# Optimization experiments

Hardware: AMD Instinct MI355X
Metric: run time of the kernel (lower is better)

Reference implementation:

```python
import jax, jax.numpy as jnp
import numpy as np
from jax.ops import segment_sum

N_NODES = 100000


def gcn_conv(x, edge_index, W, b, n_nodes):
    # PyG GCNConv: add self-loops, symmetric normalization, linear, scatter-add, bias
    src = jnp.concatenate([edge_index[0], jnp.arange(n_nodes, dtype=edge_index.dtype)])
    dst = jnp.concatenate([edge_index[1], jnp.arange(n_nodes, dtype=edge_index.dtype)])
    deg = segment_sum(jnp.ones(src.shape[0], dtype=x.dtype), dst, num_segments=n_nodes)
    dinv = jnp.where(deg > 0, jax.lax.rsqrt(deg), 0.0)
    norm = dinv[src] * dinv[dst]            # [E+N]
    h = x @ W                               # [N, out] dense GEMM first (PyG order)
    msg = h[src] * norm[:, None]            # gather + scale, [E+N, out]
    out = segment_sum(msg, dst, num_segments=n_nodes)  # scatter-add
    return out + b


def setup_inputs() -> dict:
    key = jax.random.key(0)
    k1, k2, k3, k4, k5, k6 = jax.random.split(key, 6)
    in_c, hid_c, out_c = 128, 128, 64
    n_edges = 1600000
    x = jax.random.normal(k1, (N_NODES, in_c), dtype=jnp.float32)
    edge_index = jax.random.randint(k2, (2, n_edges), 0, N_NODES, dtype=jnp.int64)
    # Glorot-ish init for weights, zeros for bias (PyG defaults)
    W1 = jax.random.normal(k3, (in_c, hid_c), dtype=jnp.float32) / np.sqrt(in_c)
    b1 = jnp.zeros((hid_c,), dtype=jnp.float32)
    W2 = jax.random.normal(k4, (hid_c, out_c), dtype=jnp.float32) / np.sqrt(hid_c)
    b2 = jnp.zeros((out_c,), dtype=jnp.float32)
    return {"x": x, "edge_index": edge_index, "W1": W1, "b1": b1, "W2": W2, "b2": b2}


def reference(x, edge_index, W1, b1, W2, b2):
    h = gcn_conv(x, edge_index, W1, b1, N_NODES)
    h = jax.nn.relu(h)
    out = gcn_conv(h, edge_index, W2, b2, N_NODES)
    return out
```

## Files before the change

### kernel.cpp

```cpp
#include <hip/hip_runtime.h>
#include <hip/hip_fp16.h>

#define NN 100000
#define NBKT 196
#define BCAP 16384

using f16x8 = __attribute__((ext_vector_type(8))) _Float16;
using f32x4 = __attribute__((ext_vector_type(4))) float;

__device__ __forceinline__ void fma4(float4& a, float s, const float4& w) {
  a.x = fmaf(s, w.x, a.x);
  a.y = fmaf(s, w.y, a.y);
  a.z = fmaf(s, w.z, a.z);
  a.w = fmaf(s, w.w, a.w);
}

__device__ __forceinline__ void add8(float* a, uint4 q) {
  const __half2* p = (const __half2*)&q;
#pragma unroll
  for (int j = 0; j < 4; ++j) {
    float2 f = __half22float2(p[j]);
    a[2 * j]     += f.x;
    a[2 * j + 1] += f.y;
  }
}

__device__ __forceinline__ unsigned packh2(float x, float y) {
  __half2 h = __floats2half2_rn(x, y);
  return *(unsigned*)&h;
}

__global__ __launch_bounds__(256) void k_binA(const int* __restrict__ e,
                                              const float* __restrict__ W1,
                                              const float* __restrict__ W2,
                                              _Float16* __restrict__ wt1,
                                              _Float16* __restrict__ wt2,
                                              int* __restrict__ gcur,
                                              unsigned int* __restrict__ tmp,
                                              int E, int nA) {
  const int b = blockIdx.x;
  const int tid = threadIdx.x;
  if (b >= nA) {
    int wb = b - nA;
    if (wb < 64) {
      int i = wb * 256 + tid;
      int n = i >> 7, k = i & 127;
      wt1[i] = (_Float16)W1[k * 128 + n];
    } else {
      int i = (wb - 64) * 256 + tid;
      int n = i >> 7, k = i & 127;
      wt2[i] = (_Float16)W2[k * 64 + n];
    }
    return;
  }
  __shared__ int cnt[256];
  __shared__ int pcur[256];
  __shared__ int sm_flag;
  cnt[tid] = 0;
  if (tid < 64) {
    int n64 = E < 64 ? E : 64;
    int odd = (tid < n64) ? e[2 * tid + 1] : 0;
    unsigned long long nz = __ballot(odd != 0);
    if (tid == 0) sm_flag = (nz == 0ull) ? 1 : 0;
  }
  __syncthreads();
  const int m = sm_flag;
  const bool pok = ((E & 1) == 0);
  const int start = b * 4096;
  int ss[16], dd[16];
#pragma unroll
  for (int k = 0; k < 8; ++k) {
    int i = start + 2 * (tid + k * 256);
    int s0 = -1, s1 = -1, d0 = 0, d1 = 0;
    if (i < E) {
      if (m) {
        if (pok) {
          int4 sp = ((const int4*)e)[i >> 1];
          int4 dp = ((const int4*)e)[(E + i) >> 1];
          s0 = sp.x; s1 = sp.z; d0 = dp.x; d1 = dp.z;
        } else {
          s0 = (int)((const long long*)e)[i];
          d0 = (int)((const long long*)e)[E + i];
          if (i + 1 < E) {
            s1 = (int)((const long long*)e)[i + 1];
            d1 = (int)((const long long*)e)[E + i + 1];
          }
        }
      } else {
        if (pok) {
          int2 sp = ((const int2*)e)[i >> 1];
          int2 dp = ((const int2*)(e + E))[i >> 1];
          s0 = sp.x; s1 = sp.y; d0 = dp.x; d1 = dp.y;
        } else {
          s0 = e[i]; d0 = e[E + i];
          if (i + 1 < E) { s1 = e[i + 1]; d1 = e[E + i + 1]; }
        }
      }
      if (i + 1 >= E) s1 = -1;
      atomicAdd(&cnt[d0 >> 9], 1);
      if (s1 >= 0) atomicAdd(&cnt[d1 >> 9], 1);
    }
    ss[2 * k] = s0; dd[2 * k] = d0;
    ss[2 * k + 1] = s1; dd[2 * k + 1] = d1;
  }
  __syncthreads();
  if (tid < NBKT && cnt[tid] > 0)
    pcur[tid] = tid * BCAP + atomicAdd(&gcur[tid], cnt[tid]);
  __syncthreads();
#pragma unroll
  for (int k = 0; k < 16; ++k) {
    if (ss[k] >= 0) {
      int bk = dd[k] >> 9;
      int p = atomicAdd(&pcur[bk], 1);
      tmp[p] = ((unsigned)ss[k] << 9) | (unsigned)(dd[k] & 511);
    }
  }
}

__global__ __launch_bounds__(256) void k_binB(const unsigned int* __restrict__ tmp,
                                              const int* __restrict__ gcur,
                                              int* __restrict__ rowptr,
                                              float* __restrict__ dinv,
                                              int* __restrict__ srcs) {
  __shared__ int sbuf[256];
  __shared__ int hist[512];
  __shared__ int lofs[512];
  const int b = blockIdx.x;
  const int tid = threadIdx.x;
  int c = (tid < NBKT) ? gcur[tid] : 0;
  sbuf[tid] = c;
  __syncthreads();
#pragma unroll
  for (int off = 1; off < 256; off <<= 1) {
    int t = (tid >= off) ? sbuf[tid - off] : 0;
    __syncthreads();
    sbuf[tid] += t;
    __syncthreads();
  }
  const int total = sbuf[255];
  const int incl = sbuf[b];
  const int base_b = (b > 0) ? sbuf[b - 1] : 0;
  const int cntb = incl - base_b;
  if (b == 0 && tid == 0) rowptr[NN] = total;
  __syncthreads();
  hist[tid] = 0;
  hist[tid + 256] = 0;
  __syncthreads();
  const int tbeg = b * BCAP;
  const int tend = tbeg + cntb;
  for (int j = tbeg + tid; j < tend; j += 256) atomicAdd(&hist[tmp[j] & 511], 1);
  __syncthreads();
  int a0 = hist[2 * tid], a1 = hist[2 * tid + 1];
  int sv = a0 + a1;
  sbuf[tid] = sv;
  __syncthreads();
#pragma unroll
  for (int off = 1; off < 256; off <<= 1) {
    int t = (tid >= off) ? sbuf[tid - off] : 0;
    __syncthreads();
    sbuf[tid] += t;
    __syncthreads();
  }
  int excl = sbuf[tid] - sv;
  lofs[2 * tid] = excl;
  lofs[2 * tid + 1] = excl + a0;
  __syncthreads();
  for (int i = tid; i < 512; i += 256) {
    int node = (b << 9) + i;
    if (node < NN) {
      rowptr[node] = base_b + lofs[i];
      dinv[node] = rsqrtf((float)(hist[i] + 1));
    }
  }
  __syncthreads();
  for (int j = tbeg + tid; j < tend; j += 256) {
    unsigned v = tmp[j];
    int p = base_b + atomicAdd(&lofs[v & 511], 1);
    srcs[p] = (int)(v >> 9);
  }
}

template <int N, bool AHALF>
__global__ __launch_bounds__(256) void k_gemm_mfma(const void* __restrict__ Av,
                                                   const _Float16* __restrict__ Wt,
                                                   const float* __restrict__ dinv,
                                                   _Float16* __restrict__ out, int M) {
  constexpr int NF = N / 16;
  __shared__ _Float16 As[64 * 136];
  __shared__ _Float16 Bs[N * 136];
  const int tid = threadIdx.x;
  const long long row0 = (long long)blockIdx.x * 64;
  if (AHALF) {
    const _Float16* A = (const _Float16*)Av;
#pragma unroll
    for (int t = 0; t < 4; ++t) {
      int i = tid + t * 256;
      int m = i >> 4, q = i & 15;
      long long row = row0 + m;
      uint4 v = make_uint4(0, 0, 0, 0);
      if (row < M) v = ((const uint4*)A)[row * 16 + q];
      *(uint4*)&As[m * 136 + q * 8] = v;
    }
  } else {
    const float* A = (const float*)Av;
#pragma unroll
    for (int t = 0; t < 8; ++t) {
      int i = tid + t * 256;
      int m = i >> 5, q = i & 31;
      long long row = row0 + m;
      float4 v = make_float4(0.f, 0.f, 0.f, 0.f);
      if (row < M) v = ((const float4*)A)[row * 32 + q];
      uint2 w2 = make_uint2(packh2(v.x, v.y), packh2(v.z, v.w));
      *(uint2*)&As[m * 136 + q * 4] = w2;
    }
  }
#pragma unroll
  for (int t = 0; t < N / 16; ++t) {
    int i = tid + t * 256;
    int n = i >> 4, q = i & 15;
    uint4 v = ((const uint4*)Wt)[i];
    *(uint4*)&Bs[n * 136 + q * 8] = v;
  }
  __syncthreads();
  const int lane = tid & 63;
  const int wrow = (tid >> 6) * 16;
  const int r = lane & 15, g = lane >> 4;
  f32x4 acc[NF] = {};
#pragma unroll
  for (int ks = 0; ks < 4; ++ks) {
    f16x8 av = *(const f16x8*)&As[(wrow + r) * 136 + ks * 32 + g * 8];
#pragma unroll
    for (int cf = 0; cf < NF; ++cf) {
      f16x8 bv = *(const f16x8*)&Bs[(cf * 16 + r) * 136 + ks * 32 + g * 8];
      acc[cf] = __builtin_amdgcn_mfma_f32_16x16x32_f16(av, bv, acc[cf], 0, 0, 0);
    }
  }
#pragma unroll
  for (int q = 0; q < 4; ++q) {
    long long row = row0 + wrow + g * 4 + q;
    if (row < M) {
      float sc = dinv[row];
#pragma unroll
      for (int cf = 0; cf < NF; ++cf)
        out[row * N + cf * 16 + r] = (_Float16)(sc * acc[cf][q]);
    }
  }
}

template <int C, bool RELU16>
__global__ __launch_bounds__(256) void k_gather_s(const int* __restrict__ rowptr,
                                                  const int* __restrict__ srcs,
                                                  const float* __restrict__ dinv,
                                                  const _Float16* __restrict__ h,
                                                  const float* __restrict__ b,
                                                  void* __restrict__ outv) {
  constexpr int LPN = C / 8;
  constexpr int NPW = 64 / LPN;
  constexpr int NPB = NPW * 4;
  const int wave = threadIdx.x >> 6;
  const int lane = threadIdx.x & 63;
  const int grp = lane / LPN;
  const int li = lane % LPN;
  const int node = blockIdx.x * NPB + wave * NPW + grp;
  if (node >= NN) return;
  const float dd = dinv[node];
  float acc[8];
  {
    uint4 q = *(const uint4*)(h + (long long)node * C + li * 8);
    const __half2* p = (const __half2*)&q;
#pragma unroll
    for (int j = 0; j < 4; ++j) {
      float2 f = __half22float2(p[j]);
      acc[2 * j]     = f.x;
      acc[2 * j + 1] = f.y;
    }
  }
  const int beg = rowptr[node], end = rowptr[node + 1];
  int e = beg;
  for (; e + 4 <= end; e += 4) {
    int s0 = srcs[e], s1 = srcs[e + 1], s2 = srcs[e + 2], s3 = srcs[e + 3];
    uint4 q0 = *(const uint4*)(h + (long long)s0 * C + li * 8);
    uint4 q1 = *(const uint4*)(h + (long long)s1 * C + li * 8);
    uint4 q2 = *(const uint4*)(h + (long long)s2 * C + li * 8);
    uint4 q3 = *(const uint4*)(h + (long long)s3 * C + li * 8);
    add8(acc, q0);
    add8(acc, q1);
    add8(acc, q2);
    add8(acc, q3);
  }
  for (; e < end; ++e) {
    uint4 q0 = *(const uint4*)(h + (long long)srcs[e] * C + li * 8);
    add8(acc, q0);
  }
  const float4* b4 = (const float4*)b;
  float4 bb0 = b4[li * 2], bb1 = b4[li * 2 + 1];
  float o[8];
  o[0] = fmaf(dd, acc[0], bb0.x);
  o[1] = fmaf(dd, acc[1], bb0.y);
  o[2] = fmaf(dd, acc[2], bb0.z);
  o[3] = fmaf(dd, acc[3], bb0.w);
  o[4] = fmaf(dd, acc[4], bb1.x);
  o[5] = fmaf(dd, acc[5], bb1.y);
  o[6] = fmaf(dd, acc[6], bb1.z);
  o[7] = fmaf(dd, acc[7], bb1.w);
  if (RELU16) {
#pragma unroll
    for (int j = 0; j < 8; ++j) o[j] = fmaxf(o[j], 0.f);
    uint4 w;
    w.x = packh2(o[0], o[1]);
    w.y = packh2(o[2], o[3]);
    w.z = packh2(o[4], o[5]);
    w.w = packh2(o[6], o[7]);
    *(uint4*)((_Float16*)outv + (long long)node * C + li * 8) = w;
  } else {
    float4* op = (float4*)((float*)outv + (long long)node * C + li * 8);
    op[0] = make_float4(o[0], o[1], o[2], o[3]);
    op[1] = make_float4(o[4], o[5], o[6], o[7]);
  }
}

__global__ void k_zero_i32(int* p, int n) {
  int i = blockIdx.x * 256 + threadIdx.x;
  if (i < n) p[i] = 0;
}

__global__ void k_detect_f(const int* __restrict__ e, int* flag, int E) {
  if (threadIdx.x == 0 && blockIdx.x == 0) {
    int n = E < 64 ? E : 64;
    int m = 1;
    for (int i = 0; i < n; ++i)
      if (e[2 * i + 1] != 0) { m = 0; break; }
    *flag = m;
  }
}

__global__ void k_deg_count(const int* __restrict__ e, const int* __restrict__ flag,
                            int* __restrict__ deg, int E) {
  int i = blockIdx.x * 256 + threadIdx.x;
  if (i >= E) return;
  int m = *flag;
  int d = m ? e[2 * (E + i)] : e[E + i];
  atomicAdd(&deg[d], 1);
}

__global__ void k_dinv_f(const int* __restrict__ deg, float* __restrict__ dinv) {
  int i = blockIdx.x * 256 + threadIdx.x;
  if (i < NN) dinv[i] = rsqrtf((float)(deg[i] + 1));
}

template <int N, bool RELU>
__global__ __launch_bounds__(256) void k_gemm_v(const float* __restrict__ A,
                                                const float* __restrict__ W,
                                                float* __restrict__ out, int M) {
  constexpr int K4 = 32;
  constexpr int N4 = N / 4;
  constexpr int CG = N4;
  constexpr int ROWS = (256 / CG) * 4;
  __shared__ float4 Wl[128 * N4];
  __shared__ float4 Xl[ROWS * K4];
  const int tid = threadIdx.x;
  const float4* W4 = (const float4*)W;
  for (int i = tid; i < 128 * N4; i += 256) Wl[i] = W4[i];
  const long long row0 = (long long)blockIdx.x * ROWS;
  const float4* A4 = (const float4*)A;
  for (int i = tid; i < ROWS * K4; i += 256) {
    int r = i >> 5;
    long long row = row0 + r;
    float4 v = make_float4(0.f, 0.f, 0.f, 0.f);
    if (row < M) v = A4[row * K4 + (i & 31)];
    if (RELU) {
      v.x = fmaxf(v.x, 0.f); v.y = fmaxf(v.y, 0.f);
      v.z = fmaxf(v.z, 0.f); v.w = fmaxf(v.w, 0.f);
    }
    Xl[i] = v;
  }
  __syncthreads();
  const int c = tid % CG;
  const int rb = (tid / CG) * 4;
  float4 a0 = make_float4(0, 0, 0, 0), a1 = a0, a2 = a0, a3 = a0;
#pragma unroll 4
  for (int k4 = 0; k4 < K4; ++k4) {
    float4 w0 = Wl[(k4 * 4 + 0) * N4 + c];
    float4 w1 = Wl[(k4 * 4 + 1) * N4 + c];
    float4 w2 = Wl[(k4 * 4 + 2) * N4 + c];
    float4 w3 = Wl[(k4 * 4 + 3) * N4 + c];
    float4 x0 = Xl[(rb + 0) * K4 + k4];
    float4 x1 = Xl[(rb + 1) * K4 + k4];
    float4 x2 = Xl[(rb + 2) * K4 + k4];
    float4 x3 = Xl[(rb + 3) * K4 + k4];
    fma4(a0, x0.x, w0); fma4(a0, x0.y, w1); fma4(a0, x0.z, w2); fma4(a0, x0.w, w3);
    fma4(a1, x1.x, w0); fma4(a1, x1.y, w1); fma4(a1, x1.z, w2); fma4(a1, x1.w, w3);
    fma4(a2, x2.x, w0); fma4(a2, x2.y, w1); fma4(a2, x2.z, w2); fma4(a2, x2.w, w3);
    fma4(a3, x3.x, w0); fma4(a3, x3.y, w1); fma4(a3, x3.z, w2); fma4(a3, x3.w, w3);
  }
  float4* O4 = (float4*)out;
  long long row = row0 + rb;
  if (row + 0 < M) O4[(row + 0) * N4 + c] = a0;
  if (row + 1 < M) O4[(row + 1) * N4 + c] = a1;
  if (row + 2 < M) O4[(row + 2) * N4 + c] = a2;
  if (row + 3 < M) O4[(row + 3) * N4 + c] = a3;
}

template <int C>
__global__ void k_self_bias(const float* __restrict__ h, const float* __restrict__ dinv,
                            const float* __restrict__ b, float* __restrict__ out) {
  constexpr int C4 = C / 4;
  int gid = blockIdx.x * 256 + threadIdx.x;
  if (gid >= NN * C4) return;
  int node = gid / C4;
  int cq = gid % C4;
  float di = dinv[node];
  float sc = di * di;
  float4 v = ((const float4*)h)[gid];
  float4 bb = ((const float4*)b)[cq];
  float4 o;
  o.x = fmaf(v.x, sc, bb.x);
  o.y = fmaf(v.y, sc, bb.y);
  o.z = fmaf(v.z, sc, bb.z);
  o.w = fmaf(v.w, sc, bb.w);
  ((float4*)out)[gid] = o;
}

template <int C>
__global__ void k_scatter(const int* __restrict__ e, const int* __restrict__ flag,
                          const float* __restrict__ dinv, const float* __restrict__ h,
                          float* __restrict__ out, int E) {
  constexpr int TPE = C / 4;
  long long gid = (long long)blockIdx.x * blockDim.x + threadIdx.x;
  int ei = (int)(gid / TPE);
  int cq = (int)(gid % TPE);
  if (ei >= E) return;
  int m = *flag;
  int s, d;
  if (m) { s = e[2 * ei]; d = e[2 * (E + ei)]; }
  else   { s = e[ei];     d = e[E + ei]; }
  float nrm = dinv[s] * dinv[d];
  float4 v = ((const float4*)h)[(long long)s * TPE + cq];
  float* op = out + (long long)d * C + (long long)cq * 4;
  unsafeAtomicAdd(op + 0, v.x * nrm);
  unsafeAtomicAdd(op + 1, v.y * nrm);
  unsafeAtomicAdd(op + 2, v.z * nrm);
  unsafeAtomicAdd(op + 3, v.w * nrm);
}

extern "C" void kernel_launch(void* const* d_in, const int* in_sizes, int n_in,
                              void* d_out, int out_size, void* d_ws, size_t ws_size,
                              hipStream_t stream) {
  const float* x  = (const float*)d_in[0];
  const int*   e  = (const int*)d_in[1];
  const float* W1 = (const float*)d_in[2];
  const float* b1 = (const float*)d_in[3];
  const float* W2 = (const float*)d_in[4];
  const float* b2 = (const float*)d_in[5];
  float* out = (float*)d_out;
  const int E = in_sizes[1] / 2;

  char* ws = (char*)d_ws;
  const size_t o_flag    = 0;
  const size_t o_dinv    = 16;
  const size_t o_rowptr  = 400016;
  const size_t o_gcur    = 800032;
  const size_t o_tmp     = 800832;
  const size_t o_srcs    = 13645888;
  const size_t o_wt1     = 20045888;
  const size_t o_wt2     = 20078656;
  const size_t o_h       = 20095040;
  const size_t o_out1    = 45695040;
  const size_t need_csr  = 71295040;

  int*      flag   = (int*)(ws + o_flag);
  float*    dinv   = (float*)(ws + o_dinv);
  int*      rowptr = (int*)(ws + o_rowptr);
  int*      gcur   = (int*)(ws + o_gcur);
  unsigned* tmp    = (unsigned*)(ws + o_tmp);
  int*      srcs   = (int*)(ws + o_srcs);
  _Float16* wt1    = (_Float16*)(ws + o_wt1);
  _Float16* wt2    = (_Float16*)(ws + o_wt2);
  _Float16* hh     = (_Float16*)(ws + o_h);
  _Float16* out1   = (_Float16*)(ws + o_out1);

  if (ws_size >= need_csr) {
    const int nA = (E + 4095) / 4096;
    hipMemsetAsync(gcur, 0, NBKT * sizeof(int), stream);
    k_binA<<<nA + 96, 256, 0, stream>>>(e, W1, W2, wt1, wt2, gcur, tmp, E, nA);
    k_binB<<<NBKT, 256, 0, stream>>>(tmp, gcur, rowptr, dinv, srcs);

    k_gemm_mfma<128, false><<<(NN + 63) / 64, 256, 0, stream>>>(x, wt1, dinv, hh, NN);
    k_gather_s<128, true><<<(NN + 15) / 16, 256, 0, stream>>>(rowptr, srcs, dinv, hh, b1, out1);

    k_gemm_mfma<64, true><<<(NN + 63) / 64, 256, 0, stream>>>(out1, wt2, dinv, hh, NN);
    k_gather_s<64, false><<<(NN + 31) / 32, 256, 0, stream>>>(rowptr, srcs, dinv, hh, b2, out);
  } else {
    int*   deg   = (int*)(ws + 400016);
    float* hF    = (float*)(ws + (1 << 20));
    float* out1F = (float*)(ws + (1 << 20) + 51200000);
    k_detect_f<<<1, 64, 0, stream>>>(e, flag, E);
    k_zero_i32<<<(NN + 255) / 256, 256, 0, stream>>>(deg, NN);
    k_deg_count<<<(E + 255) / 256, 256, 0, stream>>>(e, flag, deg, E);
    k_dinv_f<<<(NN + 255) / 256, 256, 0, stream>>>(deg, dinv);
    k_gemm_v<128, false><<<(NN + 31) / 32, 256, 0, stream>>>(x, W1, hF, NN);
    k_self_bias<128><<<(NN * 32 + 255) / 256, 256, 0, stream>>>(hF, dinv, b1, out1F);
    long long tot1 = (long long)E * 32;
    k_scatter<128><<<(int)((tot1 + 255) / 256), 256, 0, stream>>>(e, flag, dinv, hF, out1F, E);
    k_gemm_v<64, true><<<(NN + 63) / 64, 256, 0, stream>>>(out1F, W2, hF, NN);
    k_self_bias<64><<<(NN * 16 + 255) / 256, 256, 0, stream>>>(hF, dinv, b2, out);
    long long tot2 = (long long)E * 16;
    k_scatter<64><<<(int)((tot2 + 255) / 256), 256, 0, stream>>>(e, flag, dinv, hF, out, E);
  }
}
```

Measured before the change: 222.7 us.

## Store features in 16-column slices so gathers hit a smaller working set

The GEMM output and the layer-1 hidden features are now stored as 16-channel column slices, each a contiguous [NN,16] half array. The gather kernel launches one block group per slice, with 2 lanes per node, so each pass over the edges touches only a 3.2MB slice that can stay in cache instead of the full feature matrix. Index loads and output stores now use nontemporal hints. In exchange, the CSR index list is read once per slice (8x or 4x more index traffic), and the GEMM writes become more scattered.

```diff
diff --git a/kernel.cpp b/kernel.cpp
--- a/kernel.cpp
+++ b/kernel.cpp
@@ -4,9 +4,11 @@
 #define NN 100000
 #define NBKT 196
 #define BCAP 16384
+#define SLST (NN * 16)
 
 using f16x8 = __attribute__((ext_vector_type(8))) _Float16;
 using f32x4 = __attribute__((ext_vector_type(4))) float;
+using u32x4 = __attribute__((ext_vector_type(4))) unsigned;
 
 __device__ __forceinline__ void fma4(float4& a, float s, const float4& w) {
   a.x = fmaf(s, w.x, a.x);
@@ -198,7 +200,8 @@
       int m = i >> 4, q = i & 15;
       long long row = row0 + m;
       uint4 v = make_uint4(0, 0, 0, 0);
-      if (row < M) v = ((const uint4*)A)[row * 16 + q];
+      if (row < M)
+        v = *(const uint4*)(A + (size_t)(q >> 1) * SLST + row * 16 + (q & 1) * 8);
       *(uint4*)&As[m * 136 + q * 8] = v;
     }
   } else {
@@ -242,31 +245,33 @@
       float sc = dinv[row];
 #pragma unroll
       for (int cf = 0; cf < NF; ++cf)
-        out[row * N + cf * 16 + r] = (_Float16)(sc * acc[cf][q]);
+        out[(size_t)cf * SLST + row * 16 + r] = (_Float16)(sc * acc[cf][q]);
     }
   }
 }
 
 template <int C, bool RELU16>
-__global__ __launch_bounds__(256) void k_gather_s(const int* __restrict__ rowptr,
-                                                  const int* __restrict__ srcs,
-                                                  const float* __restrict__ dinv,
-                                                  const _Float16* __restrict__ h,
-                                                  const float* __restrict__ b,
-                                                  void* __restrict__ outv) {
-  constexpr int LPN = C / 8;
-  constexpr int NPW = 64 / LPN;
-  constexpr int NPB = NPW * 4;
-  const int wave = threadIdx.x >> 6;
-  const int lane = threadIdx.x & 63;
-  const int grp = lane / LPN;
-  const int li = lane % LPN;
-  const int node = blockIdx.x * NPB + wave * NPW + grp;
+__global__ __launch_bounds__(256) void k_gather_sl(const int* __restrict__ rowptr,
+                                                   const int* __restrict__ srcs,
+                                                   const float* __restrict__ dinv,
+                                                   const _Float16* __restrict__ h,
+                                                   const float* __restrict__ b,
+                                                   void* __restrict__ outv) {
+  constexpr int NSL = C / 16;
+  const int tid = threadIdx.x;
+  const int sl = (int)(blockIdx.x % NSL);
+  const int nb = (int)(blockIdx.x / NSL);
+  const int lane = tid & 63;
+  const int wave = tid >> 6;
+  const int grp = lane >> 1;
+  const int li = lane & 1;
+  const int node = nb * 128 + wave * 32 + grp;
   if (node >= NN) return;
+  const _Float16* hs = h + (size_t)sl * SLST;
   const float dd = dinv[node];
   float acc[8];
   {
-    uint4 q = *(const uint4*)(h + (long long)node * C + li * 8);
+    uint4 q = *(const uint4*)(hs + node * 16 + li * 8);
     const __half2* p = (const __half2*)&q;
 #pragma unroll
     for (int j = 0; j < 4; ++j) {
@@ -278,22 +283,27 @@
   const int beg = rowptr[node], end = rowptr[node + 1];
   int e = beg;
   for (; e + 4 <= end; e += 4) {
-    int s0 = srcs[e], s1 = srcs[e + 1], s2 = srcs[e + 2], s3 = srcs[e + 3];
-    uint4 q0 = *(const uint4*)(h + (long long)s0 * C + li * 8);
-    uint4 q1 = *(const uint4*)(h + (long long)s1 * C + li * 8);
-    uint4 q2 = *(const uint4*)(h + (long long)s2 * C + li * 8);
-    uint4 q3 = *(const uint4*)(h + (long long)s3 * C + li * 8);
+    int s0 = __builtin_nontemporal_load(srcs + e);
+    int s1 = __builtin_nontemporal_load(srcs + e + 1);
+    int s2 = __builtin_nontemporal_load(srcs + e + 2);
+    int s3 = __builtin_nontemporal_load(srcs + e + 3);
+    uint4 q0 = *(const uint4*)(hs + s0 * 16 + li * 8);
+    uint4 q1 = *(const uint4*)(hs + s1 * 16 + li * 8);
+    uint4 q2 = *(const uint4*)(hs + s2 * 16 + li * 8);
+    uint4 q3 = *(const uint4*)(hs + s3 * 16 + li * 8);
     add8(acc, q0);
     add8(acc, q1);
     add8(acc, q2);
     add8(acc, q3);
   }
   for (; e < end; ++e) {
-    uint4 q0 = *(const uint4*)(h + (long long)srcs[e] * C + li * 8);
+    int s0 = __builtin_nontemporal_load(srcs + e);
+    uint4 q0 = *(const uint4*)(hs + s0 * 16 + li * 8);
     add8(acc, q0);
   }
   const float4* b4 = (const float4*)b;
-  float4 bb0 = b4[li * 2], bb1 = b4[li * 2 + 1];
+  float4 bb0 = b4[sl * 4 + li * 2];
+  float4 bb1 = b4[sl * 4 + li * 2 + 1];
   float o[8];
   o[0] = fmaf(dd, acc[0], bb0.x);
   o[1] = fmaf(dd, acc[1], bb0.y);
@@ -306,16 +316,19 @@
   if (RELU16) {
 #pragma unroll
     for (int j = 0; j < 8; ++j) o[j] = fmaxf(o[j], 0.f);
-    uint4 w;
+    u32x4 w;
     w.x = packh2(o[0], o[1]);
     w.y = packh2(o[2], o[3]);
     w.z = packh2(o[4], o[5]);
     w.w = packh2(o[6], o[7]);
-    *(uint4*)((_Float16*)outv + (long long)node * C + li * 8) = w;
+    __builtin_nontemporal_store(
+        w, (u32x4*)((_Float16*)outv + (size_t)sl * SLST + node * 16 + li * 8));
   } else {
-    float4* op = (float4*)((float*)outv + (long long)node * C + li * 8);
-    op[0] = make_float4(o[0], o[1], o[2], o[3]);
-    op[1] = make_float4(o[4], o[5], o[6], o[7]);
+    float* op = (float*)outv + (size_t)node * C + sl * 16 + li * 8;
+    f32x4 v0 = {o[0], o[1], o[2], o[3]};
+    f32x4 v1 = {o[4], o[5], o[6], o[7]};
+    __builtin_nontemporal_store(v0, (f32x4*)op);
+    __builtin_nontemporal_store(v1, (f32x4*)(op + 4));
   }
 }
 
@@ -481,15 +494,16 @@
 
   if (ws_size >= need_csr) {
     const int nA = (E + 4095) / 4096;
-    hipMemsetAsync(gcur, 0, NBKT * sizeof(int), stream);
+    const int nNB = (NN + 127) / 128;
+    (void)hipMemsetAsync(gcur, 0, NBKT * sizeof(int), stream);
     k_binA<<<nA + 96, 256, 0, stream>>>(e, W1, W2, wt1, wt2, gcur, tmp, E, nA);
     k_binB<<<NBKT, 256, 0, stream>>>(tmp, gcur, rowptr, dinv, srcs);
 
     k_gemm_mfma<128, false><<<(NN + 63) / 64, 256, 0, stream>>>(x, wt1, dinv, hh, NN);
-    k_gather_s<128, true><<<(NN + 15) / 16, 256, 0, stream>>>(rowptr, srcs, dinv, hh, b1, out1);
+    k_gather_sl<128, true><<<nNB * 8, 256, 0, stream>>>(rowptr, srcs, dinv, hh, b1, out1);
 
     k_gemm_mfma<64, true><<<(NN + 63) / 64, 256, 0, stream>>>(out1, wt2, dinv, hh, NN);
-    k_gather_s<64, false><<<(NN + 31) / 32, 256, 0, stream>>>(rowptr, srcs, dinv, hh, b2, out);
+    k_gather_sl<64, false><<<nNB * 4, 256, 0, stream>>>(rowptr, srcs, dinv, hh, b2, out);
   } else {
     int*   deg   = (int*)(ws + 400016);
     float* hF    = (float*)(ws + (1 << 20));
```

Result: slower. 291.1 us (+30.7%).

## Fuse first GEMM into binning kernel and move degree scaling into gather

Applied to the files above, without the earlier changes.

The first GEMM no longer needs dinv, so it now runs as extra blocks of the edge-binning kernel, and that launch and the separate weight-transpose step disappear. The layer-1 gather instead applies dinv[src] per edge while it accumulates, which adds a random dinv load per edge. Weights are converted and transposed straight into shared memory inside each GEMM block. Nontemporal loads and stores are added for the srcs index stream and the gather outputs.

```diff
diff --git a/kernel.cpp b/kernel.cpp
--- a/kernel.cpp
+++ b/kernel.cpp
@@ -7,6 +7,7 @@
 
 using f16x8 = __attribute__((ext_vector_type(8))) _Float16;
 using f32x4 = __attribute__((ext_vector_type(4))) float;
+using u32x4 = __attribute__((ext_vector_type(4))) unsigned;
 
 __device__ __forceinline__ void fma4(float4& a, float s, const float4& w) {
   a.x = fmaf(s, w.x, a.x);
@@ -15,6 +16,16 @@
   a.w = fmaf(s, w.w, a.w);
 }
 
+__device__ __forceinline__ void acc8(float* a, float w, uint4 q) {
+  const __half2* p = (const __half2*)&q;
+#pragma unroll
+  for (int j = 0; j < 4; ++j) {
+    float2 f = __half22float2(p[j]);
+    a[2 * j]     = fmaf(w, f.x, a[2 * j]);
+    a[2 * j + 1] = fmaf(w, f.y, a[2 * j + 1]);
+  }
+}
+
 __device__ __forceinline__ void add8(float* a, uint4 q) {
   const __half2* p = (const __half2*)&q;
 #pragma unroll
@@ -30,41 +41,100 @@
   return *(unsigned*)&h;
 }
 
-__global__ __launch_bounds__(256) void k_binA(const int* __restrict__ e,
-                                              const float* __restrict__ W1,
-                                              const float* __restrict__ W2,
-                                              _Float16* __restrict__ wt1,
-                                              _Float16* __restrict__ wt2,
-                                              int* __restrict__ gcur,
-                                              unsigned int* __restrict__ tmp,
-                                              int E, int nA) {
+template <int N, bool AHALF, bool PRESCALE>
+__device__ __forceinline__ void gemm_body(int bid, const void* __restrict__ Av,
+                                          const float* __restrict__ W,
+                                          const float* __restrict__ dinv,
+                                          _Float16* __restrict__ out, int M,
+                                          _Float16* As, _Float16* Bs) {
+  constexpr int NF = N / 16;
+  const int tid = threadIdx.x;
+  const long long row0 = (long long)bid * 64;
+  if (AHALF) {
+    const _Float16* A = (const _Float16*)Av;
+#pragma unroll
+    for (int t = 0; t < 4; ++t) {
+      int i = tid + t * 256;
+      int m = i >> 4, q = i & 15;
+      long long row = row0 + m;
+      uint4 v = make_uint4(0, 0, 0, 0);
+      if (row < M) v = ((const uint4*)A)[row * 16 + q];
+      *(uint4*)&As[m * 136 + q * 8] = v;
+    }
+  } else {
+    const float* A = (const float*)Av;
+#pragma unroll
+    for (int t = 0; t < 8; ++t) {
+      int i = tid + t * 256;
+      int m = i >> 5, q = i & 31;
+      long long row = row0 + m;
+      float4 v = make_float4(0.f, 0.f, 0.f, 0.f);
+      if (row < M) v = ((const float4*)A)[row * 32 + q];
+      uint2 w2 = make_uint2(packh2(v.x, v.y), packh2(v.z, v.w));
+      *(uint2*)&As[m * 136 + q * 4] = w2;
+    }
+  }
+#pragma unroll
+  for (int t = 0; t < N / 2; ++t) {
+    int idx = tid + t * 256;
+    int k = idx / N, n = idx % N;
+    Bs[n * 136 + k] = (_Float16)W[idx];
+  }
+  __syncthreads();
+  const int lane = tid & 63;
+  const int wrow = (tid >> 6) * 16;
+  const int r = lane & 15, g = lane >> 4;
+  f32x4 acc[NF] = {};
+#pragma unroll
+  for (int ks = 0; ks < 4; ++ks) {
+    f16x8 av = *(const f16x8*)&As[(wrow + r) * 136 + ks * 32 + g * 8];
+#pragma unroll
+    for (int cf = 0; cf < NF; ++cf) {
+      f16x8 bv = *(const f16x8*)&Bs[(cf * 16 + r) * 136 + ks * 32 + g * 8];
+      acc[cf] = __builtin_amdgcn_mfma_f32_16x16x32_f16(av, bv, acc[cf], 0, 0, 0);
+    }
+  }
+#pragma unroll
+  for (int q = 0; q < 4; ++q) {
+    long long row = row0 + wrow + g * 4 + q;
+    if (row < M) {
+      float sc = PRESCALE ? dinv[row] : 1.0f;
+#pragma unroll
+      for (int cf = 0; cf < NF; ++cf)
+        out[row * N + cf * 16 + r] = (_Float16)(sc * acc[cf][q]);
+    }
+  }
+}
+
+__global__ __launch_bounds__(256) void k_binA_gemm(const int* __restrict__ e,
+                                                   int* __restrict__ gcur,
+                                                   unsigned int* __restrict__ tmp,
+                                                   int E, int nA,
+                                                   const float* __restrict__ x,
+                                                   const float* __restrict__ W1,
+                                                   _Float16* __restrict__ hh,
+                                                   int M) {
+  __shared__ char smem[52224];
   const int b = blockIdx.x;
   const int tid = threadIdx.x;
   if (b >= nA) {
-    int wb = b - nA;
-    if (wb < 64) {
-      int i = wb * 256 + tid;
-      int n = i >> 7, k = i & 127;
-      wt1[i] = (_Float16)W1[k * 128 + n];
-    } else {
-      int i = (wb - 64) * 256 + tid;
-      int n = i >> 7, k = i & 127;
-      wt2[i] = (_Float16)W2[k * 64 + n];
-    }
+    _Float16* As = (_Float16*)smem;
+    _Float16* Bs = (_Float16*)(smem + 64 * 136 * 2);
+    gemm_body<128, false, false>(b - nA, x, W1, nullptr, hh, M, As, Bs);
     return;
   }
-  __shared__ int cnt[256];
-  __shared__ int pcur[256];
-  __shared__ int sm_flag;
+  int* cnt = (int*)smem;
+  int* pcur = cnt + 256;
+  int* sm_flag = pcur + 256;
   cnt[tid] = 0;
   if (tid < 64) {
     int n64 = E < 64 ? E : 64;
     int odd = (tid < n64) ? e[2 * tid + 1] : 0;
     unsigned long long nz = __ballot(odd != 0);
-    if (tid == 0) sm_flag = (nz == 0ull) ? 1 : 0;
-  }
-  __syncthreads();
-  const int m = sm_flag;
+    if (tid == 0) *sm_flag = (nz == 0ull) ? 1 : 0;
+  }
+  __syncthreads();
+  const int m = *sm_flag;
   const bool pok = ((E & 1) == 0);
   const int start = b * 4096;
   int ss[16], dd[16];
@@ -117,6 +187,15 @@
   }
 }
 
+__global__ __launch_bounds__(256) void k_gemm2(const _Float16* __restrict__ A,
+                                               const float* __restrict__ W2,
+                                               const float* __restrict__ dinv,
+                                               _Float16* __restrict__ out, int M) {
+  __shared__ _Float16 As[64 * 136];
+  __shared__ _Float16 Bs[64 * 136];
+  gemm_body<64, true, true>(blockIdx.x, A, W2, dinv, out, M, As, Bs);
+}
+
 __global__ __launch_bounds__(256) void k_binB(const unsigned int* __restrict__ tmp,
                                               const int* __restrict__ gcur,
                                               int* __restrict__ rowptr,
@@ -180,88 +259,18 @@
   }
 }
 
-template <int N, bool AHALF>
-__global__ __launch_bounds__(256) void k_gemm_mfma(const void* __restrict__ Av,
-                                                   const _Float16* __restrict__ Wt,
-                                                   const float* __restrict__ dinv,
-                                                   _Float16* __restrict__ out, int M) {
-  constexpr int NF = N / 16;
-  __shared__ _Float16 As[64 * 136];
-  __shared__ _Float16 Bs[N * 136];
-  const int tid = threadIdx.x;
-  const long long row0 = (long long)blockIdx.x * 64;
-  if (AHALF) {
-    const _Float16* A = (const _Float16*)Av;
-#pragma unroll
-    for (int t = 0; t < 4; ++t) {
-      int i = tid + t * 256;
-      int m = i >> 4, q = i & 15;
-      long long row = row0 + m;
-      uint4 v = make_uint4(0, 0, 0, 0);
-      if (row < M) v = ((const uint4*)A)[row * 16 + q];
-      *(uint4*)&As[m * 136 + q * 8] = v;
-    }
-  } else {
-    const float* A = (const float*)Av;
-#pragma unroll
-    for (int t = 0; t < 8; ++t) {
-      int i = tid + t * 256;
-      int m = i >> 5, q = i & 31;
-      long long row = row0 + m;
-      float4 v = make_float4(0.f, 0.f, 0.f, 0.f);
-      if (row < M) v = ((const float4*)A)[row * 32 + q];
-      uint2 w2 = make_uint2(packh2(v.x, v.y), packh2(v.z, v.w));
-      *(uint2*)&As[m * 136 + q * 4] = w2;
-    }
-  }
-#pragma unroll
-  for (int t = 0; t < N / 16; ++t) {
-    int i = tid + t * 256;
-    int n = i >> 4, q = i & 15;
-    uint4 v = ((const uint4*)Wt)[i];
-    *(uint4*)&Bs[n * 136 + q * 8] = v;
-  }
-  __syncthreads();
-  const int lane = tid & 63;
-  const int wrow = (tid >> 6) * 16;
-  const int r = lane & 15, g = lane >> 4;
-  f32x4 acc[NF] = {};
-#pragma unroll
-  for (int ks = 0; ks < 4; ++ks) {
-    f16x8 av = *(const f16x8*)&As[(wrow + r) * 136 + ks * 32 + g * 8];
-#pragma unroll
-    for (int cf = 0; cf < NF; ++cf) {
-      f16x8 bv = *(const f16x8*)&Bs[(cf * 16 + r) * 136 + ks * 32 + g * 8];
-      acc[cf] = __builtin_amdgcn_mfma_f32_16x16x32_f16(av, bv, acc[cf], 0, 0, 0);
-    }
-  }
-#pragma unroll
-  for (int q = 0; q < 4; ++q) {
-    long long row = row0 + wrow + g * 4 + q;
-    if (row < M) {
-      float sc = dinv[row];
-#pragma unroll
-      for (int cf = 0; cf < NF; ++cf)
-        out[row * N + cf * 16 + r] = (_Float16)(sc * acc[cf][q]);
-    }
-  }
-}
-
-template <int C, bool RELU16>
-__global__ __launch_bounds__(256) void k_gather_s(const int* __restrict__ rowptr,
-                                                  const int* __restrict__ srcs,
-                                                  const float* __restrict__ dinv,
-                                                  const _Float16* __restrict__ h,
-                                                  const float* __restrict__ b,
-                                                  void* __restrict__ outv) {
-  constexpr int LPN = C / 8;
-  constexpr int NPW = 64 / LPN;
-  constexpr int NPB = NPW * 4;
+__global__ __launch_bounds__(256) void k_gather1(const int* __restrict__ rowptr,
+                                                 const int* __restrict__ srcs,
+                                                 const float* __restrict__ dinv,
+                                                 const _Float16* __restrict__ h,
+                                                 const float* __restrict__ b,
+                                                 _Float16* __restrict__ out) {
+  constexpr int C = 128;
   const int wave = threadIdx.x >> 6;
   const int lane = threadIdx.x & 63;
-  const int grp = lane / LPN;
-  const int li = lane % LPN;
-  const int node = blockIdx.x * NPB + wave * NPW + grp;
+  const int grp = lane >> 4;
+  const int li = lane & 15;
+  const int node = blockIdx.x * 16 + wave * 4 + grp;
   if (node >= NN) return;
   const float dd = dinv[node];
   float acc[8];
@@ -271,26 +280,32 @@
 #pragma unroll
     for (int j = 0; j < 4; ++j) {
       float2 f = __half22float2(p[j]);
-      acc[2 * j]     = f.x;
-      acc[2 * j + 1] = f.y;
+      acc[2 * j]     = dd * f.x;
+      acc[2 * j + 1] = dd * f.y;
     }
   }
   const int beg = rowptr[node], end = rowptr[node + 1];
   int e = beg;
   for (; e + 4 <= end; e += 4) {
-    int s0 = srcs[e], s1 = srcs[e + 1], s2 = srcs[e + 2], s3 = srcs[e + 3];
+    int s0 = __builtin_nontemporal_load(srcs + e);
+    int s1 = __builtin_nontemporal_load(srcs + e + 1);
+    int s2 = __builtin_nontemporal_load(srcs + e + 2);
+    int s3 = __builtin_nontemporal_load(srcs + e + 3);
+    float w0 = dinv[s0], w1 = dinv[s1], w2 = dinv[s2], w3 = dinv[s3];
     uint4 q0 = *(const uint4*)(h + (long long)s0 * C + li * 8);
     uint4 q1 = *(const uint4*)(h + (long long)s1 * C + li * 8);
     uint4 q2 = *(const uint4*)(h + (long long)s2 * C + li * 8);
     uint4 q3 = *(const uint4*)(h + (long long)s3 * C + li * 8);
-    add8(acc, q0);
-    add8(acc, q1);
-    add8(acc, q2);
-    add8(acc, q3);
+    acc8(acc, w0, q0);
+    acc8(acc, w1, q1);
+    acc8(acc, w2, q2);
+    acc8(acc, w3, q3);
   }
   for (; e < end; ++e) {
-    uint4 q0 = *(const uint4*)(h + (long long)srcs[e] * C + li * 8);
-    add8(acc, q0);
+    int s0 = __builtin_nontemporal_load(srcs + e);
+    float w0 = dinv[s0];
+    uint4 q0 = *(const uint4*)(h + (long long)s0 * C + li * 8);
+    acc8(acc, w0, q0);
   }
   const float4* b4 = (const float4*)b;
   float4 bb0 = b4[li * 2], bb1 = b4[li * 2 + 1];
@@ -303,20 +318,75 @@
   o[5] = fmaf(dd, acc[5], bb1.y);
   o[6] = fmaf(dd, acc[6], bb1.z);
   o[7] = fmaf(dd, acc[7], bb1.w);
-  if (RELU16) {
-#pragma unroll
-    for (int j = 0; j < 8; ++j) o[j] = fmaxf(o[j], 0.f);
-    uint4 w;
-    w.x = packh2(o[0], o[1]);
-    w.y = packh2(o[2], o[3]);
-    w.z = packh2(o[4], o[5]);
-    w.w = packh2(o[6], o[7]);
-    *(uint4*)((_Float16*)outv + (long long)node * C + li * 8) = w;
-  } else {
-    float4* op = (float4*)((float*)outv + (long long)node * C + li * 8);
-    op[0] = make_float4(o[0], o[1], o[2], o[3]);
-    op[1] = make_float4(o[4], o[5], o[6], o[7]);
-  }
+#pragma unroll
+  for (int j = 0; j < 8; ++j) o[j] = fmaxf(o[j], 0.f);
+  u32x4 w;
+  w.x = packh2(o[0], o[1]);
+  w.y = packh2(o[2], o[3]);
+  w.z = packh2(o[4], o[5]);
+  w.w = packh2(o[6], o[7]);
+  __builtin_nontemporal_store(w, (u32x4*)(out + (long long)node * C + li * 8));
+}
+
+__global__ __launch_bounds__(256) void k_gather2(const int* __restrict__ rowptr,
+                                                 const int* __restrict__ srcs,
+                                                 const float* __restrict__ dinv,
+                                                 const _Float16* __restrict__ h,
+                                                 const float* __restrict__ b,
+                                                 float* __restrict__ out) {
+  constexpr int C = 64;
+  const int wave = threadIdx.x >> 6;
+  const int lane = threadIdx.x & 63;
+  const int grp = lane >> 3;
+  const int li = lane & 7;
+  const int node = blockIdx.x * 32 + wave * 8 + grp;
+  if (node >= NN) return;
+  const float dd = dinv[node];
+  float acc[8];
+  {
+    uint4 q = *(const uint4*)(h + (long long)node * C + li * 8);
+    const __half2* p = (const __half2*)&q;
+#pragma unroll
+    for (int j = 0; j < 4; ++j) {
+      float2 f = __half22float2(p[j]);
+      acc[2 * j]     = f.x;
+      acc[2 * j + 1] = f.y;
+    }
+  }
+  const int beg = rowptr[node], end = rowptr[node + 1];
+  int e = beg;
+  for (; e + 4 <= end; e += 4) {
+    int s0 = __builtin_nontemporal_load(srcs + e);
+    int s1 = __builtin_nontemporal_load(srcs + e + 1);
+    int s2 = __builtin_nontemporal_load(srcs + e + 2);
+    int s3 = __builtin_nontemporal_load(srcs + e + 3);
+    uint4 q0 = *(const uint4*)(h + (long long)s0 * C + li * 8);
+    uint4 q1 = *(const uint4*)(h + (long long)s1 * C + li * 8);
+    uint4 q2 = *(const uint4*)(h + (long long)s2 * C + li * 8);
+    uint4 q3 = *(const uint4*)(h + (long long)s3 * C + li * 8);
+    add8(acc, q0);
+    add8(acc, q1);
+    add8(acc, q2);
+    add8(acc, q3);
+  }
+  for (; e < end; ++e) {
+    uint4 q0 = *(const uint4*)(h + (long long)__builtin_nontemporal_load(srcs + e) * C + li * 8);
+    add8(acc, q0);
+  }
+  const float4* b4 = (const float4*)b;
+  float4 bb0 = b4[li * 2], bb1 = b4[li * 2 + 1];
+  float* op = out + (long long)node * C + li * 8;
+  f32x4 v0, v1;
+  v0.x = fmaf(dd, acc[0], bb0.x);
+  v0.y = fmaf(dd, acc[1], bb0.y);
+  v0.z = fmaf(dd, acc[2], bb0.z);
+  v0.w = fmaf(dd, acc[3], bb0.w);
+  v1.x = fmaf(dd, acc[4], bb1.x);
+  v1.y = fmaf(dd, acc[5], bb1.y);
+  v1.z = fmaf(dd, acc[6], bb1.z);
+  v1.w = fmaf(dd, acc[7], bb1.w);
+  __builtin_nontemporal_store(v0, (f32x4*)op);
+  __builtin_nontemporal_store(v1, (f32x4*)(op + 4));
 }
 
 __global__ void k_zero_i32(int* p, int n) {
@@ -462,11 +532,9 @@
   const size_t o_gcur    = 800032;
   const size_t o_tmp     = 800832;
   const size_t o_srcs    = 13645888;
-  const size_t o_wt1     = 20045888;
-  const size_t o_wt2     = 20078656;
-  const size_t o_h       = 20095040;
-  const size_t o_out1    = 45695040;
-  const size_t need_csr  = 71295040;
+  const size_t o_h       = 20045888;
+  const size_t o_out1    = 45645888;
+  const size_t need_csr  = 71245888;
 
   int*      flag   = (int*)(ws + o_flag);
   float*    dinv   = (float*)(ws + o_dinv);
@@ -474,22 +542,18 @@
   int*      gcur   = (int*)(ws + o_gcur);
   unsigned* tmp    = (unsigned*)(ws + o_tmp);
   int*      srcs   = (int*)(ws + o_srcs);
-  _Float16* wt1    = (_Float16*)(ws + o_wt1);
-  _Float16* wt2    = (_Float16*)(ws + o_wt2);
   _Float16* hh     = (_Float16*)(ws + o_h);
   _Float16* out1   = (_Float16*)(ws + o_out1);
 
   if (ws_size >= need_csr) {
     const int nA = (E + 4095) / 4096;
-    hipMemsetAsync(gcur, 0, NBKT * sizeof(int), stream);
-    k_binA<<<nA + 96, 256, 0, stream>>>(e, W1, W2, wt1, wt2, gcur, tmp, E, nA);
+    const int nG = (NN + 63) / 64;
+    (void)hipMemsetAsync(gcur, 0, NBKT * sizeof(int), stream);
+    k_binA_gemm<<<nA + nG, 256, 0, stream>>>(e, gcur, tmp, E, nA, x, W1, hh, NN);
     k_binB<<<NBKT, 256, 0, stream>>>(tmp, gcur, rowptr, dinv, srcs);
-
-    k_gemm_mfma<128, false><<<(NN + 63) / 64, 256, 0, stream>>>(x, wt1, dinv, hh, NN);
-    k_gather_s<128, true><<<(NN + 15) / 16, 256, 0, stream>>>(rowptr, srcs, dinv, hh, b1, out1);
-
-    k_gemm_mfma<64, true><<<(NN + 63) / 64, 256, 0, stream>>>(out1, wt2, dinv, hh, NN);
-    k_gather_s<64, false><<<(NN + 31) / 32, 256, 0, stream>>>(rowptr, srcs, dinv, hh, b2, out);
+    k_gather1<<<(NN + 15) / 16, 256, 0, stream>>>(rowptr, srcs, dinv, hh, b1, out1);
+    k_gemm2<<<nG, 256, 0, stream>>>(out1, W2, dinv, hh, NN);
+    k_gather2<<<(NN + 31) / 32, 256, 0, stream>>>(rowptr, srcs, dinv, hh, b2, out);
   } else {
     int*   deg   = (int*)(ws + 400016);
     float* hF    = (float*)(ws + (1 << 20));
```

Result: slower. 228.9 us (+2.8%).

## Fuse layer-1 gather with layer-2 GEMM and use nontemporal index loads/stores

Applied to the files above, without the earlier changes.

The layer-1 neighbour gather (with bias, ReLU and fp16 pack) now writes its 64-row tile into shared memory, and the same block runs the layer-2 MFMA GEMM on it. This removes one kernel launch and the round trip of the 100000x128 fp16 intermediate through global memory. The edge-index reads and the final fp32 output writes now use nontemporal loads and stores to reduce cache pollution. In exchange, each fused block walks 64 nodes' neighbour lists serially in four rounds before any GEMM work, and it uses more shared memory, which can lower occupancy or latency hiding in the gather phase.

```diff
diff --git a/kernel.cpp b/kernel.cpp
--- a/kernel.cpp
+++ b/kernel.cpp
@@ -7,6 +7,7 @@
 
 using f16x8 = __attribute__((ext_vector_type(8))) _Float16;
 using f32x4 = __attribute__((ext_vector_type(4))) float;
+using u32x4 = __attribute__((ext_vector_type(4))) unsigned;
 
 __device__ __forceinline__ void fma4(float4& a, float s, const float4& w) {
   a.x = fmaf(s, w.x, a.x);
@@ -180,42 +181,27 @@
   }
 }
 
-template <int N, bool AHALF>
-__global__ __launch_bounds__(256) void k_gemm_mfma(const void* __restrict__ Av,
-                                                   const _Float16* __restrict__ Wt,
-                                                   const float* __restrict__ dinv,
-                                                   _Float16* __restrict__ out, int M) {
-  constexpr int NF = N / 16;
+__global__ __launch_bounds__(256) void k_gemm1(const float* __restrict__ A,
+                                               const _Float16* __restrict__ Wt,
+                                               const float* __restrict__ dinv,
+                                               _Float16* __restrict__ out, int M) {
+  constexpr int N = 128, NF = N / 16;
   __shared__ _Float16 As[64 * 136];
   __shared__ _Float16 Bs[N * 136];
   const int tid = threadIdx.x;
   const long long row0 = (long long)blockIdx.x * 64;
-  if (AHALF) {
-    const _Float16* A = (const _Float16*)Av;
-#pragma unroll
-    for (int t = 0; t < 4; ++t) {
-      int i = tid + t * 256;
-      int m = i >> 4, q = i & 15;
-      long long row = row0 + m;
-      uint4 v = make_uint4(0, 0, 0, 0);
-      if (row < M) v = ((const uint4*)A)[row * 16 + q];
-      *(uint4*)&As[m * 136 + q * 8] = v;
-    }
-  } else {
-    const float* A = (const float*)Av;
-#pragma unroll
-    for (int t = 0; t < 8; ++t) {
-      int i = tid + t * 256;
-      int m = i >> 5, q = i & 31;
-      long long row = row0 + m;
-      float4 v = make_float4(0.f, 0.f, 0.f, 0.f);
-      if (row < M) v = ((const float4*)A)[row * 32 + q];
-      uint2 w2 = make_uint2(packh2(v.x, v.y), packh2(v.z, v.w));
-      *(uint2*)&As[m * 136 + q * 4] = w2;
-    }
-  }
-#pragma unroll
-  for (int t = 0; t < N / 16; ++t) {
+#pragma unroll
+  for (int t = 0; t < 8; ++t) {
+    int i = tid + t * 256;
+    int m = i >> 5, q = i & 31;
+    long long row = row0 + m;
+    float4 v = make_float4(0.f, 0.f, 0.f, 0.f);
+    if (row < M) v = ((const float4*)A)[row * 32 + q];
+    uint2 w2 = make_uint2(packh2(v.x, v.y), packh2(v.z, v.w));
+    *(uint2*)&As[m * 136 + q * 4] = w2;
+  }
+#pragma unroll
+  for (int t = 0; t < 8; ++t) {
     int i = tid + t * 256;
     int n = i >> 4, q = i & 15;
     uint4 v = ((const uint4*)Wt)[i];
@@ -247,21 +233,122 @@
   }
 }
 
-template <int C, bool RELU16>
-__global__ __launch_bounds__(256) void k_gather_s(const int* __restrict__ rowptr,
-                                                  const int* __restrict__ srcs,
-                                                  const float* __restrict__ dinv,
-                                                  const _Float16* __restrict__ h,
-                                                  const float* __restrict__ b,
-                                                  void* __restrict__ outv) {
-  constexpr int LPN = C / 8;
-  constexpr int NPW = 64 / LPN;
-  constexpr int NPB = NPW * 4;
+__global__ __launch_bounds__(256) void k_g1g2(const int* __restrict__ rowptr,
+                                              const int* __restrict__ srcs,
+                                              const float* __restrict__ dinv,
+                                              const _Float16* __restrict__ h,
+                                              const float* __restrict__ b1,
+                                              const _Float16* __restrict__ wt2,
+                                              _Float16* __restrict__ h2, int M) {
+  __shared__ _Float16 As[64 * 136];
+  __shared__ _Float16 Bs[64 * 136];
+  const int tid = threadIdx.x;
+  const int lane = tid & 63;
+  const int wave = tid >> 6;
+  const long long row0 = (long long)blockIdx.x * 64;
+#pragma unroll
+  for (int t = 0; t < 4; ++t) {
+    int i = tid + t * 256;
+    int n = i >> 4, q = i & 15;
+    uint4 v = ((const uint4*)wt2)[i];
+    *(uint4*)&Bs[n * 136 + q * 8] = v;
+  }
+  const int grp = lane >> 4;
+  const int li = lane & 15;
+  const float4* b4 = (const float4*)b1;
+  const float4 bb0 = b4[li * 2], bb1 = b4[li * 2 + 1];
+#pragma unroll
+  for (int rnd = 0; rnd < 4; ++rnd) {
+    const int m = rnd * 16 + wave * 4 + grp;
+    const long long node = row0 + m;
+    uint4 w = make_uint4(0, 0, 0, 0);
+    if (node < M) {
+      const float dd = dinv[node];
+      float acc[8];
+      {
+        uint4 q0 = *(const uint4*)(h + node * 128 + li * 8);
+        const __half2* p = (const __half2*)&q0;
+#pragma unroll
+        for (int j = 0; j < 4; ++j) {
+          float2 f = __half22float2(p[j]);
+          acc[2 * j]     = f.x;
+          acc[2 * j + 1] = f.y;
+        }
+      }
+      const int beg = rowptr[node], end = rowptr[node + 1];
+      int e = beg;
+      for (; e + 4 <= end; e += 4) {
+        int s0 = __builtin_nontemporal_load(srcs + e);
+        int s1 = __builtin_nontemporal_load(srcs + e + 1);
+        int s2 = __builtin_nontemporal_load(srcs + e + 2);
+        int s3 = __builtin_nontemporal_load(srcs + e + 3);
+        uint4 q0 = *(const uint4*)(h + (long long)s0 * 128 + li * 8);
+        uint4 q1 = *(const uint4*)(h + (long long)s1 * 128 + li * 8);
+        uint4 q2 = *(const uint4*)(h + (long long)s2 * 128 + li * 8);
+        uint4 q3 = *(const uint4*)(h + (long long)s3 * 128 + li * 8);
+        add8(acc, q0);
+        add8(acc, q1);
+        add8(acc, q2);
+        add8(acc, q3);
+      }
+      for (; e < end; ++e) {
+        int s0 = __builtin_nontemporal_load(srcs + e);
+        uint4 q0 = *(const uint4*)(h + (long long)s0 * 128 + li * 8);
+        add8(acc, q0);
+      }
+      float o[8];
+      o[0] = fmaxf(fmaf(dd, acc[0], bb0.x), 0.f);
+      o[1] = fmaxf(fmaf(dd, acc[1], bb0.y), 0.f);
+      o[2] = fmaxf(fmaf(dd, acc[2], bb0.z), 0.f);
+      o[3] = fmaxf(fmaf(dd, acc[3], bb0.w), 0.f);
+      o[4] = fmaxf(fmaf(dd, acc[4], bb1.x), 0.f);
+      o[5] = fmaxf(fmaf(dd, acc[5], bb1.y), 0.f);
+      o[6] = fmaxf(fmaf(dd, acc[6], bb1.z), 0.f);
+      o[7] = fmaxf(fmaf(dd, acc[7], bb1.w), 0.f);
+      w.x = packh2(o[0], o[1]);
+      w.y = packh2(o[2], o[3]);
+      w.z = packh2(o[4], o[5]);
+      w.w = packh2(o[6], o[7]);
+    }
+    *(uint4*)&As[m * 136 + li * 8] = w;
+  }
+  __syncthreads();
+  const int r = lane & 15, g = lane >> 4;
+  const int wrow = wave * 16;
+  f32x4 acc2[4] = {};
+#pragma unroll
+  for (int ks = 0; ks < 4; ++ks) {
+    f16x8 av = *(const f16x8*)&As[(wrow + r) * 136 + ks * 32 + g * 8];
+#pragma unroll
+    for (int cf = 0; cf < 4; ++cf) {
+      f16x8 bv = *(const f16x8*)&Bs[(cf * 16 + r) * 136 + ks * 32 + g * 8];
+      acc2[cf] = __builtin_amdgcn_mfma_f32_16x16x32_f16(av, bv, acc2[cf], 0, 0, 0);
+    }
+  }
+#pragma unroll
+  for (int q = 0; q < 4; ++q) {
+    long long row = row0 + wrow + g * 4 + q;
+    if (row < M) {
+      float sc = dinv[row];
+#pragma unroll
+      for (int cf = 0; cf < 4; ++cf)
+        h2[row * 64 + cf * 16 + r] = (_Float16)(sc * acc2[cf][q]);
+    }
+  }
+}
+
+__global__ __launch_bounds__(256) void k_gather2(const int* __restrict__ rowptr,
+                                                 const int* __restrict__ srcs,
+                                                 const float* __restrict__ dinv,
+                                                 const _Float16* __restrict__ h,
+                                                 const float* __restrict__ b,
+                                                 float* __restrict__ out) {
+  constexpr int C = 64;
   const int wave = threadIdx.x >> 6;
   const int lane = threadIdx.x & 63;
-  const int grp = lane / LPN;
-  const int li = lane % LPN;
-  const int node = blockIdx.x * NPB + wave * NPW + grp;
+  const int grp = lane >> 3;
+  const int li = lane & 7;
+  const int node = blockIdx.x * 32 + wave * 8 + grp;
   if (node >= NN) return;
   const float dd = dinv[node];
   float acc[8];
@@ -278,7 +365,10 @@
   const int beg = rowptr[node], end = rowptr[node + 1];
   int e = beg;
   for (; e + 4 <= end; e += 4) {
-    int s0 = srcs[e], s1 = srcs[e + 1], s2 = srcs[e + 2], s3 = srcs[e + 3];
+    int s0 = __builtin_nontemporal_load(srcs + e);
+    int s1 = __builtin_nontemporal_load(srcs + e + 1);
+    int s2 = __builtin_nontemporal_load(srcs + e + 2);
+    int s3 = __builtin_nontemporal_load(srcs + e + 3);
     uint4 q0 = *(const uint4*)(h + (long long)s0 * C + li * 8);
     uint4 q1 = *(const uint4*)(h + (long long)s1 * C + li * 8);
     uint4 q2 = *(const uint4*)(h + (long long)s2 * C + li * 8);
@@ -289,34 +379,23 @@
     add8(acc, q3);
   }
   for (; e < end; ++e) {
-    uint4 q0 = *(const uint4*)(h + (long long)srcs[e] * C + li * 8);
+    uint4 q0 = *(const uint4*)(h + (long long)__builtin_nontemporal_load(srcs + e) * C + li * 8);
     add8(acc, q0);
   }
   const float4* b4 = (const float4*)b;
   float4 bb0 = b4[li * 2], bb1 = b4[li * 2 + 1];
-  float o[8];
-  o[0] = fmaf(dd, acc[0], bb0.x);
-  o[1] = fmaf(dd, acc[1], bb0.y);
-  o[2] = fmaf(dd, acc[2], bb0.z);
-  o[3] = fmaf(dd, acc[3], bb0.w);
-  o[4] = fmaf(dd, acc[4], bb1.x);
-  o[5] = fmaf(dd, acc[5], bb1.y);
-  o[6] = fmaf(dd, acc[6], bb1.z);
-  o[7] = fmaf(dd, acc[7], bb1.w);
-  if (RELU16) {
-#pragma unroll
-    for (int j = 0; j < 8; ++j) o[j] = fmaxf(o[j], 0.f);
-    uint4 w;
-    w.x = packh2(o[0], o[1]);
-    w.y = packh2(o[2], o[3]);
-    w.z = packh2(o[4], o[5]);
-    w.w = packh2(o[6], o[7]);
-    *(uint4*)((_Float16*)outv + (long long)node * C + li * 8) = w;
-  } else {
-    float4* op = (float4*)((float*)outv + (long long)node * C + li * 8);
-    op[0] = make_float4(o[0], o[1], o[2], o[3]);
-    op[1] = make_float4(o[4], o[5], o[6], o[7]);
-  }
+  float* op = out + (long long)node * C + li * 8;
+  f32x4 v0, v1;
+  v0.x = fmaf(dd, acc[0], bb0.x);
+  v0.y = fmaf(dd, acc[1], bb0.y);
+  v0.z = fmaf(dd, acc[2], bb0.z);
+  v0.w = fmaf(dd, acc[3], bb0.w);
+  v1.x = fmaf(dd, acc[4], bb1.x);
+  v1.y = fmaf(dd, acc[5], bb1.y);
+  v1.z = fmaf(dd, acc[6], bb1.z);
+  v1.w = fmaf(dd, acc[7], bb1.w);
+  __builtin_nontemporal_store(v0, (f32x4*)op);
+  __builtin_nontemporal_store(v1, (f32x4*)(op + 4));
 }
 
 __global__ void k_zero_i32(int* p, int n) {
@@ -465,8 +544,8 @@
   const size_t o_wt1     = 20045888;
   const size_t o_wt2     = 20078656;
   const size_t o_h       = 20095040;
-  const size_t o_out1    = 45695040;
-  const size_t need_csr  = 71295040;
+  const size_t o_h2      = 45695040;
+  const size_t need_csr  = 58495040;
 
   int*      flag   = (int*)(ws + o_flag);
   float*    dinv   = (float*)(ws + o_dinv);
@@ -477,19 +556,17 @@
   _Float16* wt1    = (_Float16*)(ws + o_wt1);
   _Float16* wt2    = (_Float16*)(ws + o_wt2);
   _Float16* hh     = (_Float16*)(ws + o_h);
-  _Float16* out1   = (_Float16*)(ws + o_out1);
+  _Float16* h2     = (_Float16*)(ws + o_h2);
 
   if (ws_size >= need_csr) {
     const int nA = (E + 4095) / 4096;
-    hipMemsetAsync(gcur, 0, NBKT * sizeof(int), stream);
+    const int nG = (NN + 63) / 64;
+    (void)hipMemsetAsync(gcur, 0, NBKT * sizeof(int), stream);
     k_binA<<<nA + 96, 256, 0, stream>>>(e, W1, W2, wt1, wt2, gcur, tmp, E, nA);
     k_binB<<<NBKT, 256, 0, stream>>>(tmp, gcur, rowptr, dinv, srcs);
-
-    k_gemm_mfma<128, false><<<(NN + 63) / 64, 256, 0, stream>>>(x, wt1, dinv, hh, NN);
-    k_gather_s<128, true><<<(NN + 15) / 16, 256, 0, stream>>>(rowptr, srcs, dinv, hh, b1, out1);
-
-    k_gemm_mfma<64, true><<<(NN + 63) / 64, 256, 0, stream>>>(out1, wt2, dinv, hh, NN);
-    k_gather_s<64, false><<<(NN + 31) / 32, 256, 0, stream>>>(rowptr, srcs, dinv, hh, b2, out);
+    k_gemm1<<<nG, 256, 0, stream>>>(x, wt1, dinv, hh, NN);
+    k_g1g2<<<nG, 256, 0, stream>>>(rowptr, srcs, dinv, hh, b1, wt2, h2, NN);
+    k_gather2<<<(NN + 31) / 32, 256, 0, stream>>>(rowptr, srcs, dinv, h2, b2, out);
   } else {
     int*   deg   = (int*)(ws + 400016);
     float* hF    = (float*)(ws + (1 << 20));
```

After: 224.7 us. About the same (+0.9%).
